# Kernel tuning notes

Hardware: AMD Instinct MI355X
Metric: run time of the kernel (lower is better)

The kernel has to match this reference:

```python
import jax, jax.numpy as jnp
import numpy as np

# ---- static HashEncoder config (matches __init__ defaults) ----
D = 3            # input_dim
L = 16           # num_levels
C = 2            # level_dim
BASE = 16.0      # base_resolution (isotropic)
SCALE = 2.0      # per_level_scale (isotropic)
MAX_PARAMS = 2 ** 19  # log2_hashmap_size = 19

_base = np.full(D, BASE, dtype=np.float64)
_pls = np.full(D, SCALE, dtype=np.float64)
_offsets = [0]
_res = []
_off = 0
for i in range(L):
    r = np.ceil(_base * _pls ** i)
    _res.append(r.astype(np.int64))
    _off += int(min(MAX_PARAMS, np.prod(r)))
    _offsets.append(_off)
TOTAL_PARAMS = _off  # 7,114,752

# spatial-hash primes (instant-ngp convention; prime for dim 0 is 1)
PRIMES = np.array([1, 2654435761, 805459861], dtype=np.uint32)
# corner bit patterns for the 2^D = 8 cube corners, shape [8, D]
BITS = np.array([[(c >> d) & 1 for d in range(D)] for c in range(2 ** D)], dtype=np.uint32)
BITS_MASK = BITS.astype(bool)


def _encode_level(x01, embeddings, l):
    """x01: [B, D] normalized coords in [0, 1]; returns [B, C]."""
    scale = (_base * _pls ** l - 1.0).astype(np.float32)        # per-dim grid scale
    res = _res[l]                                               # per-dim resolution
    level_size = _offsets[l + 1] - _offsets[l]
    pos = x01 * scale + 0.5                                     # [B, D]
    pos_grid = jnp.floor(pos)
    frac = pos - pos_grid                                       # [B, D] in [0,1)
    pg = pos_grid.astype(jnp.uint32)                            # [B, D]
    corners = pg[:, None, :] + BITS[None]                       # [B, 8, D]
    # trilinear weights: prod over dims of frac (bit=1) or 1-frac (bit=0)
    w = jnp.prod(jnp.where(BITS_MASK[None], frac[:, None, :], 1.0 - frac[:, None, :]), axis=-1)  # [B, 8]
    if int(np.prod(res)) > level_size:
        # hashed level: xor of per-dim (coord * prime), mod table size
        h = corners * PRIMES[None, None, :]
        idx = (h[..., 0] ^ h[..., 1] ^ h[..., 2]) % jnp.uint32(level_size)
    else:
        # dense level: row-major stride indexing
        stride = np.array([1, res[0], res[0] * res[1]], dtype=np.uint32)
        idx = jnp.sum(corners * stride[None, None, :], axis=-1)  # [B, 8]
    g = embeddings[_offsets[l] + idx.astype(jnp.int32)]          # [B, 8, C] gather
    return jnp.sum(w[..., None] * g, axis=1)                     # [B, C]


def setup_inputs() -> dict:
    key = jax.random.key(0)
    k1, k2 = jax.random.split(key)
    B = 1048576
    inputs = jax.random.uniform(k1, (B, D), dtype=jnp.float32, minval=-1.0, maxval=1.0)
    # reset_parameters(): uniform(-0.1, 0.1)
    embeddings = jax.random.uniform(k2, (TOTAL_PARAMS, C), dtype=jnp.float32, minval=-0.1, maxval=0.1)
    return {"inputs": inputs, "embeddings": embeddings}


def reference(inputs, embeddings):
    # forward(inputs, size=1): normalize [-1,1] -> [0,1]
    x01 = (inputs + 1.0) * 0.5
    outs = [_encode_level(x01, embeddings, l) for l in range(L)]
    return jnp.concatenate(outs, axis=-1)  # [B, L*C] = [B, 32]
```

## Files before the change

### kernel.cpp

```cpp
#include <hip/hip_runtime.h>


static constexpr uint32_t P1 = 2654435761u;
static constexpr uint32_t P2 = 805459861u;
static constexpr uint32_t NPARAMS = 7114752u;

__device__ inline uint32_t bf16_bits(float f) {
    uint32_t u = __float_as_uint(f);
    return (u + 0x7FFFu + ((u >> 16) & 1u)) >> 16;
}

__global__ __launch_bounds__(256) void convert_bf16(
    const float* __restrict__ emb, uint32_t* __restrict__ tab)
{
    const uint32_t i = blockIdx.x * 256u + threadIdx.x;
    const float4 v = ((const float4*)emb)[i];
    uint2 o;
    o.x = bf16_bits(v.x) | (bf16_bits(v.y) << 16);
    o.y = bf16_bits(v.z) | (bf16_bits(v.w) << 16);
    ((uint2*)tab)[i] = o;
}

__global__ __launch_bounds__(256) void enc_level(
    const float* __restrict__ inp,
    const uint32_t* __restrict__ tab,
    float2* __restrict__ stage,
    int npoints)
{
    const uint32_t l = blockIdx.y;
    const uint32_t p = blockIdx.x * 256u + threadIdx.x;
    if (p >= (uint32_t)npoints) return;

    const float x01 = (inp[p * 3u + 0u] + 1.0f) * 0.5f;
    const float y01 = (inp[p * 3u + 1u] + 1.0f) * 0.5f;
    const float z01 = (inp[p * 3u + 2u] + 1.0f) * 0.5f;

    const uint32_t res = 16u << l;
    const float scale = (float)(res - 1u);

    const float posx = x01 * scale + 0.5f;
    const float posy = y01 * scale + 0.5f;
    const float posz = z01 * scale + 0.5f;

    const float fgx = floorf(posx), fgy = floorf(posy), fgz = floorf(posz);
    const float fx = posx - fgx, fy = posy - fgy, fz = posz - fgz;
    const uint32_t gx = (uint32_t)fgx, gy = (uint32_t)fgy, gz = (uint32_t)fgz;

    uint32_t off;
    if (l >= 3u)      off = 299008u + (l - 3u) * 524288u;
    else if (l == 2u) off = 36864u;
    else if (l == 1u) off = 4096u;
    else              off = 0u;
    const bool hashed = (l >= 3u);
    const uint32_t s = 4u + (hashed ? 0u : l);

    const float wx[2] = {1.0f - fx, fx};
    const float wy[2] = {1.0f - fy, fy};
    const float wz[2] = {1.0f - fz, fz};

    uint32_t gp[8];
    float    w[8];
#pragma unroll
    for (int c = 0; c < 8; ++c) {
        const uint32_t bx = (uint32_t)c & 1u;
        const uint32_t by = ((uint32_t)c >> 1) & 1u;
        const uint32_t bz = ((uint32_t)c >> 2) & 1u;
        const uint32_t cx = gx + bx, cy = gy + by, cz = gz + bz;
        const uint32_t hidx = (cx ^ (cy * P1) ^ (cz * P2)) & 524287u;
        const uint32_t didx = cx + (cy << s) + (cz << (2u * s));
        const uint32_t idx  = hashed ? hidx : didx;
        w[c]  = wx[bx] * wy[by] * wz[bz];
        gp[c] = tab[off + idx];
    }

    float sx = 0.0f, sy = 0.0f;
#pragma unroll
    for (int c = 0; c < 8; ++c) {
        const float ex = __uint_as_float(gp[c] << 16);
        const float ey = __uint_as_float(gp[c] & 0xFFFF0000u);
        sx = fmaf(w[c], ex, sx);
        sy = fmaf(w[c], ey, sy);
    }

    stage[(size_t)l * (uint32_t)npoints + p] = make_float2(sx, sy);
}

__global__ __launch_bounds__(256) void transpose_out(
    const float2* __restrict__ stage, float* __restrict__ out, int npoints)
{
    const uint32_t p = blockIdx.x * 256u + threadIdx.x;
    if (p >= (uint32_t)npoints) return;
    float2 v[16];
#pragma unroll
    for (int l = 0; l < 16; ++l)
        v[l] = stage[(size_t)l * (uint32_t)npoints + p];
    float4* o = (float4*)(out + (size_t)p * 32u);
#pragma unroll
    for (int k = 0; k < 8; ++k)
        o[k] = make_float4(v[2 * k].x, v[2 * k].y, v[2 * k + 1].x, v[2 * k + 1].y);
}

__global__ __launch_bounds__(256) void hashenc_fwd(
    const float* __restrict__ inp, const float* __restrict__ emb,
    float* __restrict__ out, int npoints)
{
    const uint32_t tid = blockIdx.x * 256u + threadIdx.x;
    const uint32_t p = tid >> 4, l = tid & 15u;
    if (p >= (uint32_t)npoints) return;
    const float x01 = (inp[p * 3u + 0u] + 1.0f) * 0.5f;
    const float y01 = (inp[p * 3u + 1u] + 1.0f) * 0.5f;
    const float z01 = (inp[p * 3u + 2u] + 1.0f) * 0.5f;
    const uint32_t res = 16u << l;
    const float scale = (float)(res - 1u);
    const float posx = x01 * scale + 0.5f, posy = y01 * scale + 0.5f, posz = z01 * scale + 0.5f;
    const float fgx = floorf(posx), fgy = floorf(posy), fgz = floorf(posz);
    const float fx = posx - fgx, fy = posy - fgy, fz = posz - fgz;
    const uint32_t gx = (uint32_t)fgx, gy = (uint32_t)fgy, gz = (uint32_t)fgz;
    uint32_t off;
    if (l >= 3u)      off = 299008u + (l - 3u) * 524288u;
    else if (l == 2u) off = 36864u;
    else if (l == 1u) off = 4096u;
    else              off = 0u;
    const bool hashed = (l >= 3u);
    const uint32_t s = 4u + (hashed ? 0u : l);
    const float wx[2] = {1.0f - fx, fx}, wy[2] = {1.0f - fy, fy}, wz[2] = {1.0f - fz, fz};
    float2 g[8]; float w[8];
#pragma unroll
    for (int c = 0; c < 8; ++c) {
        const uint32_t bx = (uint32_t)c & 1u, by = ((uint32_t)c >> 1) & 1u, bz = ((uint32_t)c >> 2) & 1u;
        const uint32_t cx = gx + bx, cy = gy + by, cz = gz + bz;
        const uint32_t hidx = (cx ^ (cy * P1) ^ (cz * P2)) & 524287u;
        const uint32_t didx = cx + (cy << s) + (cz << (2u * s));
        const uint32_t idx  = hashed ? hidx : didx;
        w[c] = wx[bx] * wy[by] * wz[bz];
        g[c] = *(const float2*)(emb + 2u * (off + idx));
    }
    float sx = 0.0f, sy = 0.0f;
#pragma unroll
    for (int c = 0; c < 8; ++c) { sx = fmaf(w[c], g[c].x, sx); sy = fmaf(w[c], g[c].y, sy); }
    *(float2*)(out + (size_t)p * 32u + (size_t)l * 2u) = make_float2(sx, sy);
}

extern "C" void kernel_launch(void* const* d_in, const int* in_sizes, int n_in,
                              void* d_out, int out_size, void* d_ws, size_t ws_size,
                              hipStream_t stream) {
    const float* inp = (const float*)d_in[0];
    const float* emb = (const float*)d_in[1];
    float* out = (float*)d_out;
    const int npoints = in_sizes[0] / 3;

    const size_t tab_bytes = (size_t)NPARAMS * 4u;
    const size_t stage_bytes = (size_t)npoints * 16u * 8u;
    const size_t need = tab_bytes + stage_bytes;

    if (ws_size >= need && (npoints & 255) == 0) {
        uint32_t* tab = (uint32_t*)d_ws;
        float2* stage = (float2*)((char*)d_ws + tab_bytes);

        const int conv_units = (int)(NPARAMS * 2u / 4u);
        convert_bf16<<<(conv_units + 255) / 256, 256, 0, stream>>>(emb, tab);

        dim3 g1(npoints / 256, 16);
        enc_level<<<g1, 256, 0, stream>>>(inp, tab, stage, npoints);

        transpose_out<<<npoints / 256, 256, 0, stream>>>(stage, out, npoints);
    } else {
        const int total = npoints * 16;
        hashenc_fwd<<<(total + 255) / 256, 256, 0, stream>>>(inp, emb, out, npoints);
    }
}
```

Before: 674.2 us.

## Pair x-adjacent corner gathers into 8-byte loads and stage transpose through LDS

```diff
diff --git a/kernel.cpp b/kernel.cpp
--- a/kernel.cpp
+++ b/kernel.cpp
@@ -4,6 +4,7 @@
 static constexpr uint32_t P1 = 2654435761u;
 static constexpr uint32_t P2 = 805459861u;
 static constexpr uint32_t NPARAMS = 7114752u;
+static constexpr uint32_t HMASK = 524287u;
 
 __device__ inline uint32_t bf16_bits(float f) {
     uint32_t u = __float_as_uint(f);
@@ -54,50 +55,88 @@
     const bool hashed = (l >= 3u);
     const uint32_t s = 4u + (hashed ? 0u : l);
 
-    const float wx[2] = {1.0f - fx, fx};
+    const float wx0 = 1.0f - fx, wx1 = fx;
     const float wy[2] = {1.0f - fy, fy};
     const float wz[2] = {1.0f - fz, fz};
 
-    uint32_t gp[8];
-    float    w[8];
-#pragma unroll
-    for (int c = 0; c < 8; ++c) {
-        const uint32_t bx = (uint32_t)c & 1u;
-        const uint32_t by = ((uint32_t)c >> 1) & 1u;
-        const uint32_t bz = ((uint32_t)c >> 2) & 1u;
-        const uint32_t cx = gx + bx, cy = gy + by, cz = gz + bz;
-        const uint32_t hidx = (cx ^ (cy * P1) ^ (cz * P2)) & 524287u;
-        const uint32_t didx = cx + (cy << s) + (cz << (2u * s));
-        const uint32_t idx  = hashed ? hidx : didx;
-        w[c]  = wx[bx] * wy[by] * wz[bz];
-        gp[c] = tab[off + idx];
+    uint32_t yzc[4];
+    if (hashed) {
+        const uint32_t hy0 = gy * P1, hy1 = hy0 + P1;
+        const uint32_t hz0 = gz * P2, hz1 = hz0 + P2;
+        yzc[0] = hy0 ^ hz0; yzc[1] = hy1 ^ hz0;
+        yzc[2] = hy0 ^ hz1; yzc[3] = hy1 ^ hz1;
+    } else {
+        const uint32_t dy0 = gy << s, dy1 = dy0 + (1u << s);
+        const uint32_t dz0 = gz << (2u * s), dz1 = dz0 + (1u << (2u * s));
+        yzc[0] = dy0 + dz0; yzc[1] = dy1 + dz0;
+        yzc[2] = dy0 + dz1; yzc[3] = dy1 + dz1;
+    }
+
+    const bool gx_odd = (gx & 1u) != 0u;
+
+    uint32_t idxA[4], idxB[4];
+#pragma unroll
+    for (int c = 0; c < 4; ++c) {
+        if (hashed) {
+            idxA[c] = (gx ^ yzc[c]) & HMASK;
+            idxB[c] = ((gx + 1u) ^ yzc[c]) & HMASK;
+        } else {
+            idxA[c] = gx + yzc[c];
+            idxB[c] = idxA[c] + 1u;
+        }
+    }
+
+    uint2 pr[4];
+#pragma unroll
+    for (int c = 0; c < 4; ++c)
+        pr[c] = *(const uint2*)(tab + off + (idxA[c] & ~1u));
+
+    uint32_t vBo[4];
+    if (gx_odd) {
+#pragma unroll
+        for (int c = 0; c < 4; ++c)
+            vBo[c] = tab[off + idxB[c]];
     }
 
     float sx = 0.0f, sy = 0.0f;
 #pragma unroll
-    for (int c = 0; c < 8; ++c) {
-        const float ex = __uint_as_float(gp[c] << 16);
-        const float ey = __uint_as_float(gp[c] & 0xFFFF0000u);
-        sx = fmaf(w[c], ex, sx);
-        sy = fmaf(w[c], ey, sy);
+    for (int c = 0; c < 4; ++c) {
+        const uint32_t lo = idxA[c] & 1u;
+        const uint32_t vA = lo ? pr[c].y : pr[c].x;
+        const uint32_t vBe = lo ? pr[c].x : pr[c].y;
+        const uint32_t vB = gx_odd ? vBo[c] : vBe;
+        const float wyz = wy[c & 1] * wz[c >> 1];
+        const float eAx = __uint_as_float(vA << 16);
+        const float eAy = __uint_as_float(vA & 0xFFFF0000u);
+        const float eBx = __uint_as_float(vB << 16);
+        const float eBy = __uint_as_float(vB & 0xFFFF0000u);
+        sx = fmaf(wyz, fmaf(wx0, eAx, wx1 * eBx), sx);
+        sy = fmaf(wyz, fmaf(wx0, eAy, wx1 * eBy), sy);
     }
 
     stage[(size_t)l * (uint32_t)npoints + p] = make_float2(sx, sy);
 }
 
 __global__ __launch_bounds__(256) void transpose_out(
-    const float2* __restrict__ stage, float* __restrict__ out, int npoints)
-{
-    const uint32_t p = blockIdx.x * 256u + threadIdx.x;
-    if (p >= (uint32_t)npoints) return;
-    float2 v[16];
+    const float2* __restrict__ stage, float4* __restrict__ out4, int npoints)
+{
+    __shared__ float2 t[256][17];
+    const uint32_t p0 = blockIdx.x * 256u;
+    const uint32_t tid = threadIdx.x;
+
 #pragma unroll
     for (int l = 0; l < 16; ++l)
-        v[l] = stage[(size_t)l * (uint32_t)npoints + p];
-    float4* o = (float4*)(out + (size_t)p * 32u);
-#pragma unroll
-    for (int k = 0; k < 8; ++k)
-        o[k] = make_float4(v[2 * k].x, v[2 * k].y, v[2 * k + 1].x, v[2 * k + 1].y);
+        t[tid][l] = stage[(size_t)l * (uint32_t)npoints + p0 + tid];
+    __syncthreads();
+
+#pragma unroll
+    for (int k = 0; k < 8; ++k) {
+        const uint32_t f = (uint32_t)k * 256u + tid;
+        const uint32_t p = f >> 3, c = f & 7u;
+        const float2 a = t[p][2u * c];
+        const float2 b = t[p][2u * c + 1u];
+        out4[(size_t)(p0 + p) * 8u + c] = make_float4(a.x, a.y, b.x, b.y);
+    }
 }
 
 __global__ __launch_bounds__(256) void hashenc_fwd(
@@ -129,7 +168,7 @@
     for (int c = 0; c < 8; ++c) {
         const uint32_t bx = (uint32_t)c & 1u, by = ((uint32_t)c >> 1) & 1u, bz = ((uint32_t)c >> 2) & 1u;
         const uint32_t cx = gx + bx, cy = gy + by, cz = gz + bz;
-        const uint32_t hidx = (cx ^ (cy * P1) ^ (cz * P2)) & 524287u;
+        const uint32_t hidx = (cx ^ (cy * P1) ^ (cz * P2)) & HMASK;
         const uint32_t didx = cx + (cy << s) + (cz << (2u * s));
         const uint32_t idx  = hashed ? hidx : didx;
         w[c] = wx[bx] * wy[by] * wz[bz];
@@ -163,7 +202,7 @@
         dim3 g1(npoints / 256, 16);
         enc_level<<<g1, 256, 0, stream>>>(inp, tab, stage, npoints);
 
-        transpose_out<<<npoints / 256, 256, 0, stream>>>(stage, out, npoints);
+        transpose_out<<<npoints / 256, 256, 0, stream>>>(stage, (float4*)out, npoints);
     } else {
         const int total = npoints * 16;
         hashenc_fwd<<<(total + 255) / 256, 256, 0, stream>>>(inp, emb, out, npoints);
```

Measured after the change: 584.5 us. -13.3%, faster.
